# Performance work log

Measured on AMD Instinct MI355X. Metric: run time of the kernel, lower is better.

The kernel has to match this reference:

```python
import jax, jax.numpy as jnp
import numpy as np

IN, H1, H2, H3, H4, OUT = 512, 2048, 2048, 1024, 512, 1


def setup_inputs() -> dict:
    key = jax.random.key(0)
    ks = jax.random.split(key, 12)
    def lin(k, fan_in, fan_out):
        # torch Linear default init: U(-1/sqrt(fan_in), 1/sqrt(fan_in))
        bound = 1.0 / np.sqrt(fan_in)
        k1, k2 = jax.random.split(k)
        W = jax.random.uniform(k1, (fan_out, fan_in), jnp.float32, -bound, bound)
        b = jax.random.uniform(k2, (fan_out,), jnp.float32, -bound, bound)
        return W, b
    x = jax.random.normal(ks[0], (16384, IN), jnp.float32)
    cross_w = jnp.ones((IN,), jnp.float32)   # init.constant_(1.0)
    cross_b = jnp.zeros((IN,), jnp.float32)  # init.constant_(0.0)
    W1, b1 = lin(ks[1], IN, H1)
    W2, b2 = lin(ks[2], H1, H2)
    W3, b3 = lin(ks[3], H2, H3)
    W4, b4 = lin(ks[4], H3, H4)
    Wo, bo = lin(ks[5], H4, OUT)
    return {"x": x, "cross_w": cross_w, "cross_b": cross_b,
            "W1": W1, "b1": b1, "W2": W2, "b2": b2,
            "W3": W3, "b3": b3, "W4": W4, "b4": b4,
            "Wo": Wo, "bo": bo}


def reference(x, cross_w, cross_b, W1, b1, W2, b2, W3, b3, W4, b4, Wo, bo):
    # Cross layer: bmm(x0[...,None], x[...,None,:]) . w == x0 * (x . w)
    # (mathematically identical, avoids the O(f^2) outer product)
    xw = x @ cross_w                         # [B]
    h = x * xw[:, None] + cross_b + x        # [B, IN]
    h = jax.nn.relu(h @ W1.T + b1)           # [B, H1]
    h = jax.nn.relu(h @ W2.T + b2)           # [B, H2]
    h = jax.nn.relu(h @ W3.T + b3)           # [B, H3]
    h = jax.nn.relu(h @ W4.T + b4)           # [B, H4]
    return h @ Wo.T + bo                     # [B, OUT]
```

## Files before the change

kernel.cpp:

```cpp
#include <hip/hip_runtime.h>


#define BK 64

typedef __bf16 bf16x8 __attribute__((ext_vector_type(8)));
typedef float  f32x4  __attribute__((ext_vector_type(4)));
typedef unsigned short u16x4 __attribute__((ext_vector_type(4)));

__device__ __forceinline__ unsigned short f2bf(float f) {
    unsigned int u = __builtin_bit_cast(unsigned int, f);
    u += 0x7fffu + ((u >> 16) & 1u);
    return (unsigned short)(u >> 16);
}

__device__ __forceinline__ void async16(const void* g, void* l) {
    __builtin_amdgcn_global_load_lds(
        (const __attribute__((address_space(1))) unsigned int*)g,
        (__attribute__((address_space(3))) unsigned int*)l,
        16, 0, 0);
}

#define BAR()   __builtin_amdgcn_s_barrier()
#define LGKM0() asm volatile("s_waitcnt lgkmcnt(0)" ::: "memory")
#define VMW(n)  asm volatile("s_waitcnt vmcnt(" #n ")" ::: "memory")

#define RDA(REGION) do { _Pragma("unroll") \
    for (int f = 0; f < 4; ++f) { \
        af[f][0] = *(const bf16x8*)(lds + (REGION) + aRd + f * 1024 + c0); \
        af[f][1] = *(const bf16x8*)(lds + (REGION) + aRd + f * 1024 + c1); } } while (0)

#define RDB(DST, REGION) do { _Pragma("unroll") \
    for (int c = 0; c < 2; ++c) { \
        DST[c][0] = *(const bf16x8*)(lds + (REGION) + bRd + c * 1024 + c0); \
        DST[c][1] = *(const bf16x8*)(lds + (REGION) + bRd + c * 1024 + c1); } } while (0)

#define MM16(HA, HB, AF, BF) do { \
    __builtin_amdgcn_s_setprio(1); \
    _Pragma("unroll") for (int f = 0; f < 4; ++f) \
    _Pragma("unroll") for (int c = 0; c < 2; ++c) { \
        acc[HA][f][HB][c] = __builtin_amdgcn_mfma_f32_16x16x32_bf16( \
            AF[f][0], BF[c][0], acc[HA][f][HB][c], 0, 0, 0); \
        acc[HA][f][HB][c] = __builtin_amdgcn_mfma_f32_16x16x32_bf16( \
            AF[f][1], BF[c][1], acc[HA][f][HB][c], 0, 0, 0); } \
    __builtin_amdgcn_s_setprio(0); } while (0)

__global__ __launch_bounds__(512, 2)
void gemm8_bt_bias_relu(const unsigned short* __restrict__ A,
                        const unsigned short* __restrict__ B,
                        const float* __restrict__ bias,
                        unsigned short* __restrict__ C,
                        int M, int N, int K)
{
    __shared__ __align__(16) unsigned short L[65536];
    unsigned short* lds = L;

    constexpr int RA00 = 0,     RA01 = 8192,  RA10 = 16384, RA11 = 24576;
    constexpr int RB00 = 32768, RB01 = 40960, RB10 = 49152, RB11 = 57344;

    const int tid  = threadIdx.x;
    const int lane = tid & 63;
    const int wave = tid >> 6;
    const int quad = lane >> 4;
    const int l16  = lane & 15;
    const int wr   = wave >> 2;
    const int wc   = wave & 3;

    const int bm = blockIdx.x * 256;
    const int bn = blockIdx.y * 256;

    const int lrow = tid >> 3;
    const int cswz = ((tid & 7) ^ (lrow & 7)) * 8;
    const int tid8 = tid * 8;
    const size_t rstep64 = (size_t)64 * K;
    const unsigned short* gaL = A + (size_t)(bm + lrow) * K + cswz;
    const unsigned short* gaH = gaL + (size_t)128 * K;
    const unsigned short* gbL = B + (size_t)(bn + lrow) * K + cswz;
    const unsigned short* gbH = gbL + (size_t)128 * K;

    auto stage = [&](const unsigned short* g, int region, int ko) {
        async16(g + ko,           lds + region + tid8);
        async16(g + rstep64 + ko, lds + region + 4096 + tid8);
    };

    const int xa = l16 & 7;
    const int c0 = (quad ^ xa) * 8;
    const int c1 = ((quad ^ 4) ^ xa) * 8;
    const int aRd = (64 * wr + l16) * BK;
    const int bRd = (32 * wc + l16) * BK;

    f32x4 acc[2][4][2][2] = {};
    bf16x8 af[4][2], bfl[2][2], bfh[2][2];

    stage(gaL, RA00, 0);
    stage(gbL, RB00, 0);
    stage(gbH, RB01, 0);
    stage(gaH, RA01, 0);
    stage(gaL, RA10, 64);
    stage(gbL, RB10, 64);
    stage(gbH, RB11, 64);
    VMW(6);
    BAR();

    const int nIter = K >> 7;
    for (int i = 0; i < nIter; ++i) {
        const int k1 = (2 * i + 1) << 6;
        int k2 = (2 * i + 2) << 6; if (k2 >= K) k2 -= K;
        int k3 = (2 * i + 3) << 6; if (k3 >= K) k3 -= K;

        RDA(RA00); RDB(bfl, RB00);
        stage(gaH, RA11, k1);
        BAR(); LGKM0();
        MM16(0, 0, af, bfl);
        BAR();

        RDB(bfh, RB01);
        stage(gaL, RA00, k2);
        BAR(); LGKM0();
        MM16(0, 1, af, bfh);
        BAR();

        RDA(RA01);
        stage(gbL, RB00, k2);
        BAR(); LGKM0();
        MM16(1, 1, af, bfh);
        BAR();

        stage(gbH, RB01, k2);
        BAR();
        MM16(1, 0, af, bfl);
        VMW(6);
        BAR();

        RDA(RA10); RDB(bfl, RB10);
        stage(gaH, RA01, k2);
        BAR(); LGKM0();
        MM16(0, 0, af, bfl);
        BAR();

        RDB(bfh, RB11);
        stage(gaL, RA10, k3);
        BAR(); LGKM0();
        MM16(0, 1, af, bfh);
        BAR();

        RDA(RA11);
        stage(gbL, RB10, k3);
        BAR(); LGKM0();
        MM16(1, 1, af, bfh);
        BAR();

        stage(gbH, RB11, k3);
        BAR();
        MM16(1, 0, af, bfl);
        VMW(6);
        BAR();
    }
    VMW(0);

    float bv[2][2];
#pragma unroll
    for (int hb = 0; hb < 2; ++hb)
#pragma unroll
        for (int c = 0; c < 2; ++c)
            bv[hb][c] = bias[bn + hb * 128 + wc * 32 + c * 16 + l16];

#pragma unroll
    for (int ha = 0; ha < 2; ++ha)
#pragma unroll
    for (int f = 0; f < 4; ++f) {
        const int row0 = bm + ha * 128 + wr * 64 + f * 16 + quad * 4;
#pragma unroll
        for (int hb = 0; hb < 2; ++hb)
#pragma unroll
        for (int c = 0; c < 2; ++c) {
            const int col = bn + hb * 128 + wc * 32 + c * 16 + l16;
#pragma unroll
            for (int r = 0; r < 4; ++r) {
                float v = fmaxf(acc[ha][f][hb][c][r] + bv[hb][c], 0.0f);
                C[(size_t)(row0 + r) * N + col] = f2bf(v);
            }
        }
    }
}

__global__ __launch_bounds__(256, 2)
void gemm_bt_head(const unsigned short* __restrict__ A,
                  const unsigned short* __restrict__ B,
                  const float* __restrict__ bias,
                  const float* __restrict__ Wo,
                  float* __restrict__ out,
                  int M, int N, int K)
{
    constexpr int BN = 128;
    constexpr int JT = 4;
    __shared__ __align__(16) unsigned short As[128 * BK];
    __shared__ __align__(16) unsigned short Bs[BN * BK];

    const int tid  = threadIdx.x;
    const int lane = tid & 63;
    const int wave = tid >> 6;
    const int quad = lane >> 4;
    const int l16  = lane & 15;

    const int bm = blockIdx.x * 128;
    const int bn = blockIdx.y * BN;
    const int wm = (wave & 1) * 64;
    const int wn = (wave >> 1) * 64;

    const int lrow = tid >> 3;
    const int gcol = ((tid & 7) ^ (lrow & 7)) * 8;

    const unsigned short* gaBase = A + (size_t)(bm + lrow) * K + gcol;
    const unsigned short* gbBase = B + (size_t)(bn + lrow) * K + gcol;

    unsigned short* lA = As + tid * 8;
    unsigned short* lB = Bs + tid * 8;

    const int xa = l16 & 7;
    const unsigned short* As_w = As + (wm + l16) * BK;
    const unsigned short* Bs_w = Bs + (wn + l16) * BK;
    const int c0 = (quad ^ xa) * 8;
    const int c1 = ((quad ^ 4) ^ xa) * 8;

    f32x4 acc[4][JT] = {};

    for (int k0 = 0; k0 < K; k0 += BK) {
#pragma unroll
        for (int i = 0; i < 4; ++i)
            async16(gaBase + (size_t)(i * 32) * K + k0, lA + i * 2048);
#pragma unroll
        for (int i = 0; i < JT; ++i)
            async16(gbBase + (size_t)(i * 32) * K + k0, lB + i * 2048);
        __syncthreads();

#pragma unroll
        for (int kk = 0; kk < 2; ++kk) {
            const int cs = kk ? c1 : c0;
            bf16x8 af[4], bfr[JT];
#pragma unroll
            for (int i = 0; i < 4; ++i)  af[i]  = *(const bf16x8*)(As_w + i * 16 * BK + cs);
#pragma unroll
            for (int j = 0; j < JT; ++j) bfr[j] = *(const bf16x8*)(Bs_w + j * 16 * BK + cs);
#pragma unroll
            for (int i = 0; i < 4; ++i)
#pragma unroll
                for (int j = 0; j < JT; ++j)
                    acc[i][j] = __builtin_amdgcn_mfma_f32_16x16x32_bf16(
                        af[i], bfr[j], acc[i][j], 0, 0, 0);
        }
        __syncthreads();
    }

    float bv[JT], wov[JT];
#pragma unroll
    for (int j = 0; j < JT; ++j) {
        const int col = bn + wn + j * 16 + l16;
        bv[j]  = bias[col];
        wov[j] = Wo[col];
    }

#pragma unroll
    for (int i = 0; i < 4; ++i) {
#pragma unroll
        for (int r = 0; r < 4; ++r) {
            float ws = 0.f;
#pragma unroll
            for (int j = 0; j < JT; ++j) {
                float v = acc[i][j][r] + bv[j];
                v = fmaxf(v, 0.0f);
                ws += v * wov[j];
            }
#pragma unroll
            for (int off = 8; off > 0; off >>= 1)
                ws += __shfl_xor(ws, off, 64);
            if (l16 == 0) {
                const int row = bm + wm + i * 16 + quad * 4 + r;
                atomicAdd(&out[row], ws);
            }
        }
    }
}

__global__ __launch_bounds__(256)
void prep_kernel(const float* __restrict__ x, const float* __restrict__ cw,
                 const float* __restrict__ cb, unsigned short* __restrict__ h0,
                 const float* __restrict__ s1, const float* __restrict__ s2,
                 const float* __restrict__ s3, const float* __restrict__ s4,
                 unsigned short* __restrict__ d1, unsigned short* __restrict__ d2,
                 unsigned short* __restrict__ d3, unsigned short* __restrict__ d4,
                 const float* __restrict__ bo, float* __restrict__ out)
{
    const int b = blockIdx.x;
    if (b < 7680) {
        long t = (long)b * 256 + threadIdx.x;
        const float* s; unsigned short* d; long off;
        if (t < 262144L)       { s = s1; d = d1; off = t; }
        else if (t < 1310720L) { s = s2; d = d2; off = t - 262144L; }
        else if (t < 1835008L) { s = s3; d = d3; off = t - 1310720L; }
        else                   { s = s4; d = d4; off = t - 1835008L; }
        f32x4 f = *(const f32x4*)(s + off * 4);
        u16x4 o;
#pragma unroll
        for (int i = 0; i < 4; ++i) o[i] = f2bf(f[i]);
        *(u16x4*)(d + off * 4) = o;
    } else if (b < 11776) {
        const int row  = (b - 7680) * 4 + (threadIdx.x >> 6);
        const int lane = threadIdx.x & 63;
        const float* xr = x + (size_t)row * 512;
        float xv[8];
        float s = 0.f;
#pragma unroll
        for (int i = 0; i < 8; ++i) {
            const int c = lane + i * 64;
            xv[i] = xr[c];
            s += xv[i] * cw[c];
        }
#pragma unroll
        for (int off = 32; off > 0; off >>= 1) s += __shfl_down(s, off, 64);
        s = __shfl(s, 0, 64);
        unsigned short* hr = h0 + (size_t)row * 512;
#pragma unroll
        for (int i = 0; i < 8; ++i) {
            const int c = lane + i * 64;
            hr[c] = f2bf(xv[i] * s + cb[c] + xv[i]);
        }
    } else {
        const int t = (b - 11776) * 256 + threadIdx.x;
        out[t] = bo[0];
    }
}

extern "C" void kernel_launch(void* const* d_in, const int* in_sizes, int n_in,
                              void* d_out, int out_size, void* d_ws, size_t ws_size,
                              hipStream_t stream)
{
    const float* x  = (const float*)d_in[0];
    const float* cw = (const float*)d_in[1];
    const float* cb = (const float*)d_in[2];
    const float* W1 = (const float*)d_in[3];  const float* b1 = (const float*)d_in[4];
    const float* W2 = (const float*)d_in[5];  const float* b2 = (const float*)d_in[6];
    const float* W3 = (const float*)d_in[7];  const float* b3 = (const float*)d_in[8];
    const float* W4 = (const float*)d_in[9];  const float* b4 = (const float*)d_in[10];
    const float* Wo = (const float*)d_in[11]; const float* bo = (const float*)d_in[12];
    float* out = (float*)d_out;

    char* p = (char*)d_ws;
    unsigned short* wb1 = (unsigned short*)p; p += (size_t)2048 * 512  * 2;
    unsigned short* wb2 = (unsigned short*)p; p += (size_t)2048 * 2048 * 2;
    unsigned short* wb3 = (unsigned short*)p; p += (size_t)1024 * 2048 * 2;
    unsigned short* wb4 = (unsigned short*)p; p += (size_t)512  * 1024 * 2;
    unsigned short* actA = (unsigned short*)p; p += (size_t)16384 * 2048 * 2;
    unsigned short* actB = (unsigned short*)p;

    prep_kernel<<<11840, 256, 0, stream>>>(x, cw, cb, actA,
                                           W1, W2, W3, W4, wb1, wb2, wb3, wb4,
                                           bo, out);

    gemm8_bt_bias_relu<<<dim3(64, 8), 512, 0, stream>>>(actA, wb1, b1, actB, 16384, 2048, 512);
    gemm8_bt_bias_relu<<<dim3(64, 8), 512, 0, stream>>>(actB, wb2, b2, actA, 16384, 2048, 2048);
    gemm8_bt_bias_relu<<<dim3(64, 4), 512, 0, stream>>>(actA, wb3, b3, actB, 16384, 1024, 2048);
    gemm_bt_head<<<dim3(128, 4), 256, 0, stream>>>(actB, wb4, b4, Wo, out, 16384, 512, 1024);
}
```

Before: 359.0 us.

## Halve GEMM main-loop barriers and overlap LDS fragment reads with MFMA

Restructures the double-buffered GEMM main loop to use one barrier per phase instead of two, and drops the explicit lgkmcnt(0) waits. LDS fragment reads for the next sub-tile are now issued right after the current MFMA block, so the compiler can overlap them with the matrix work. LDS read addresses become precomputed byte base pointers plus constant offsets, which cuts per-read address arithmetic. The risk is a race on the LDS regions being restaged, since ordering now depends on compiler-inserted waitcnts before each barrier, and extra register pressure from keeping fragments live longer.

```diff
diff --git a/kernel.cpp b/kernel.cpp
--- a/kernel.cpp
+++ b/kernel.cpp
@@ -21,18 +21,17 @@
 }
 
 #define BAR()   __builtin_amdgcn_s_barrier()
-#define LGKM0() asm volatile("s_waitcnt lgkmcnt(0)" ::: "memory")
 #define VMW(n)  asm volatile("s_waitcnt vmcnt(" #n ")" ::: "memory")
 
-#define RDA(REGION) do { _Pragma("unroll") \
+#define RDA(RBYTE) do { _Pragma("unroll") \
     for (int f = 0; f < 4; ++f) { \
-        af[f][0] = *(const bf16x8*)(lds + (REGION) + aRd + f * 1024 + c0); \
-        af[f][1] = *(const bf16x8*)(lds + (REGION) + aRd + f * 1024 + c1); } } while (0)
-
-#define RDB(DST, REGION) do { _Pragma("unroll") \
+        af[f][0] = *(const bf16x8*)(aB0 + (RBYTE) + f * 2048); \
+        af[f][1] = *(const bf16x8*)(aB1 + (RBYTE) + f * 2048); } } while (0)
+
+#define RDB(DST, RBYTE) do { _Pragma("unroll") \
     for (int c = 0; c < 2; ++c) { \
-        DST[c][0] = *(const bf16x8*)(lds + (REGION) + bRd + c * 1024 + c0); \
-        DST[c][1] = *(const bf16x8*)(lds + (REGION) + bRd + c * 1024 + c1); } } while (0)
+        DST[c][0] = *(const bf16x8*)(bB0 + (RBYTE) + c * 2048); \
+        DST[c][1] = *(const bf16x8*)(bB1 + (RBYTE) + c * 2048); } } while (0)
 
 #define MM16(HA, HB, AF, BF) do { \
     __builtin_amdgcn_s_setprio(1); \
@@ -56,6 +55,8 @@
 
     constexpr int RA00 = 0,     RA01 = 8192,  RA10 = 16384, RA11 = 24576;
     constexpr int RB00 = 32768, RB01 = 40960, RB10 = 49152, RB11 = 57344;
+    constexpr int A00b = 0, A01b = 16384, A10b = 32768, A11b = 49152;
+    constexpr int B00b = 0, B01b = 16384, B10b = 32768, B11b = 49152;
 
     const int tid  = threadIdx.x;
     const int lane = tid & 63;
@@ -87,6 +88,10 @@
     const int c1 = ((quad ^ 4) ^ xa) * 8;
     const int aRd = (64 * wr + l16) * BK;
     const int bRd = (32 * wc + l16) * BK;
+    const char* aB0 = (const char*)L + 2 * (aRd + c0);
+    const char* aB1 = (const char*)L + 2 * (aRd + c1);
+    const char* bB0 = (const char*)L + 65536 + 2 * (bRd + c0);
+    const char* bB1 = (const char*)L + 65536 + 2 * (bRd + c1);
 
     f32x4 acc[2][4][2][2] = {};
     bf16x8 af[4][2], bfl[2][2], bfh[2][2];
@@ -107,51 +112,43 @@
         int k2 = (2 * i + 2) << 6; if (k2 >= K) k2 -= K;
         int k3 = (2 * i + 3) << 6; if (k3 >= K) k3 -= K;
 
-        RDA(RA00); RDB(bfl, RB00);
+        RDA(A00b); RDB(bfl, B00b);
+        MM16(0, 0, af, bfl);
+        RDB(bfh, B01b);
         stage(gaH, RA11, k1);
-        BAR(); LGKM0();
+        BAR();
+
+        MM16(0, 1, af, bfh);
+        RDA(A01b);
+        stage(gaL, RA00, k2);
+        BAR();
+
+        MM16(1, 1, af, bfh);
+        stage(gbL, RB00, k2);
+        BAR();
+
+        MM16(1, 0, af, bfl);
+        stage(gbH, RB01, k2);
+        VMW(6);
+        BAR();
+
+        RDA(A10b); RDB(bfl, B10b);
         MM16(0, 0, af, bfl);
-        BAR();
-
-        RDB(bfh, RB01);
-        stage(gaL, RA00, k2);
-        BAR(); LGKM0();
+        RDB(bfh, B11b);
+        stage(gaH, RA01, k2);
+        BAR();
+
         MM16(0, 1, af, bfh);
-        BAR();
-
-        RDA(RA01);
-        stage(gbL, RB00, k2);
-        BAR(); LGKM0();
+        RDA(A11b);
+        stage(gaL, RA10, k3);
+        BAR();
+
         MM16(1, 1, af, bfh);
-        BAR();
-
-        stage(gbH, RB01, k2);
-        BAR();
+        stage(gbL, RB10, k3);
+        BAR();
+
         MM16(1, 0, af, bfl);
-        VMW(6);
-        BAR();
-
-        RDA(RA10); RDB(bfl, RB10);
-        stage(gaH, RA01, k2);
-        BAR(); LGKM0();
-        MM16(0, 0, af, bfl);
-        BAR();
-
-        RDB(bfh, RB11);
-        stage(gaL, RA10, k3);
-        BAR(); LGKM0();
-        MM16(0, 1, af, bfh);
-        BAR();
-
-        RDA(RA11);
-        stage(gbL, RB10, k3);
-        BAR(); LGKM0();
-        MM16(1, 1, af, bfh);
-        BAR();
-
         stage(gbH, RB11, k3);
-        BAR();
-        MM16(1, 0, af, bfl);
         VMW(6);
         BAR();
     }
```

Measured after the change: 344.2 us. 4.1% less time.
